# Kernel tuning notes

Measured on AMD Instinct MI355X. Metric: run time of the kernel, lower is better.

The kernel has to match this reference:

```python
import jax, jax.numpy as jnp
import numpy as np

BETA = 0.5

def setup_inputs() -> dict:
    key = jax.random.key(0)
    ks = jax.random.split(key, 10)
    B, H = 4096, 200
    ITEM, REGION = 100000, 1000
    D, HID = 128, 64  # embed_size, hidden_size
    half = D // 2
    history = jax.random.randint(ks[0], (B, H), 0, ITEM)
    target = jax.random.randint(ks[1], (B,), 0, ITEM)
    history_region = jax.random.randint(ks[2], (B, H), 0, REGION)
    target_region = jax.random.randint(ks[3], (B,), 0, REGION)
    W_hist = jax.random.normal(ks[4], (ITEM, half), jnp.float32) * 0.01
    W_tgt = jax.random.normal(ks[5], (ITEM, half), jnp.float32) * 0.01
    W_reg = jax.random.normal(ks[6], (REGION, half), jnp.float32) * 0.01
    W1 = jax.random.normal(ks[7], (D, HID), jnp.float32) * (1.0 / np.sqrt(D))
    b1 = jnp.zeros((HID,), jnp.float32)
    W2 = jax.random.normal(ks[8], (HID,), jnp.float32) * (1.0 / np.sqrt(HID))
    return {"history": history, "target": target,
            "history_region": history_region, "target_region": target_region,
            "W_hist": W_hist, "W_tgt": W_tgt, "W_reg": W_reg,
            "W1": W1, "b1": b1, "W2": W2}

def reference(history, target, history_region, target_region,
              W_hist, W_tgt, W_reg, W1, b1, W2):
    # gather + concat: [B,H,D] and [B,D]
    h = jnp.concatenate([W_hist[history], W_reg[history_region]], axis=-1)
    t = jnp.concatenate([W_tgt[target], W_reg[target_region]], axis=-1)
    inp = h * t[:, None, :]                      # [B,H,D]
    r1 = jax.nn.relu(inp @ W1 + b1)              # [B,H,HID] (dropout = identity at eval)
    logits = r1 @ W2                             # [B,H]
    mask = (history != target[:, None]).astype(logits.dtype)
    exp_A = jnp.exp(logits) * mask               # [B,H]
    exp_sum = jnp.sum(exp_A, axis=-1) ** BETA    # [B], beta-power normalization
    attn = exp_A / exp_sum[:, None]              # [B,H]
    pred = jnp.einsum('bhd,bd->b', h * attn[..., None], t)
    return jax.nn.sigmoid(pred)
```

## Files before the change

kernel.cpp:

```cpp
#include <hip/hip_runtime.h>
#include <math.h>

#define NB        4096
#define NH        200
#define HIST_ROWS 100000
#define REG_ROWS  1000
#define NTILES    13

typedef __attribute__((ext_vector_type(4))) int   int4i;

#define SA 2048.0f
#define SB 16384.0f
#define ST 2048.0f
#define INV_LOGIT (1.0f / (SA * SB))
#define INV_S     (1.0f / (SA * ST))

__device__ __forceinline__ int q8(float x, float s) {
    return __float2int_rn(fminf(fmaxf(x * s, -127.f), 127.f));
}
__device__ __forceinline__ int pack4(float a, float b, float c, float d, float s) {
    const int x0 = q8(a, s), x1 = q8(b, s), x2 = q8(c, s), x3 = q8(d, s);
    return (x0 & 255) | ((x1 & 255) << 8) | ((x2 & 255) << 16) | (x3 << 24);
}

__global__ __launch_bounds__(256) void prep_i8(
    const float* __restrict__ Wh, const float* __restrict__ Wr,
    const float* __restrict__ W1,
    unsigned char* __restrict__ tab, float* __restrict__ W1F2)
{
    for (int i = blockIdx.x * blockDim.x + threadIdx.x; i < 10240;
         i += gridDim.x * blockDim.x) {
        const int chunk = i >> 4, j = i & 15;
        const int frag = chunk >> 6, nt = frag >> 1, ks = frag & 1;
        const int c = chunk & 63, q = c >> 4, l = c & 15;
        W1F2[i] = (nt < 4) ? W1[(ks * 64 + q * 16 + j) * 64 + nt * 16 + l] : 0.f;
    }
    const int total = (HIST_ROWS + REG_ROWS) * 16;
    const int HE    = HIST_ROWS * 16;
    unsigned* dst = (unsigned*)tab;
    for (int i = blockIdx.x * blockDim.x + threadIdx.x; i < total;
         i += gridDim.x * blockDim.x) {
        const float4 v = (i < HE) ? ((const float4*)Wh)[i]
                                  : ((const float4*)Wr)[i - HE];
        dst[i] = (unsigned)pack4(v.x, v.y, v.z, v.w, SA);
    }
}

__global__ __launch_bounds__(256, 3) void nais_wl(
    const int*   __restrict__ history,
    const int*   __restrict__ target,
    const int*   __restrict__ history_region,
    const int*   __restrict__ target_region,
    const float* __restrict__ W_tgt,
    const float* __restrict__ W_reg,
    const float* __restrict__ b1,
    const float* __restrict__ W2,
    const unsigned char* __restrict__ tab,
    const float* __restrict__ W1F2,
    float*       __restrict__ out)
{
    __shared__ __align__(16) int Bw[4 * 640 * 4];

    const int tid  = threadIdx.x;
    const int lane = tid & 63, wv = tid >> 6;
    const int b    = blockIdx.x * 4 + wv;
    const int l15  = lane & 15, quad = lane >> 4;
    const int r_sel = l15 & 3;
    const int bNH  = b * NH;
    const int q16  = quad * 16;

    const int tgt  = target[b];
    const int treg = target_region[b];
    const float* tW = W_tgt + (size_t)tgt * 64;
    const float* rW = W_reg + (size_t)treg * 64;

    int4i*       Bst = (int4i*)Bw + wv * 640;
    const int4i* Bp  = (const int4i*)Bw + wv * 640;

    int4i sAh0, sAr0, sAh1, sAr1, sAh2, sAr2;
    int   mIh0, mIr0, mIh1, mIr1, mIh2, mIr2;

#define LOADIDX(S, T) do {                                                    \
        int j_ = (T) * 16 + l15;                                              \
        if (j_ >= NH) j_ = NH - 1;             \
        mIh##S = history[bNH + j_];                                           \
        mIr##S = history_region[bNH + j_];                                    \
    } while (0)

#define GATH(S) do {                                                          \
        sAh##S = *(const int4i*)(tab + (size_t)mIh##S * 64 + q16);            \
        sAr##S = *(const int4i*)(tab + (size_t)(HIST_ROWS + mIr##S) * 64 + q16); \
    } while (0)

    LOADIDX(0, 0); GATH(0);
    LOADIDX(1, 1); GATH(1);
    LOADIDX(2, 2); GATH(2);

    #pragma unroll
    for (int v = 0; v < 10; ++v) {
        const int ks = v & 1;
        const float4* tp = (const float4*)((ks ? rW : tW) + q16);
        const float4 t0 = tp[0], t1 = tp[1], t2 = tp[2], t3 = tp[3];
        int4i ob;
        if (v < 8) {
            const float4* wp = (const float4*)(W1F2 + (v * 64 + lane) * 16);
            const float4 w0 = wp[0], w1 = wp[1], w2 = wp[2], w3 = wp[3];
            ob.x = pack4(w0.x * t0.x, w0.y * t0.y, w0.z * t0.z, w0.w * t0.w, SB);
            ob.y = pack4(w1.x * t1.x, w1.y * t1.y, w1.z * t1.z, w1.w * t1.w, SB);
            ob.z = pack4(w2.x * t2.x, w2.y * t2.y, w2.z * t2.z, w2.w * t2.w, SB);
            ob.w = pack4(w3.x * t3.x, w3.y * t3.y, w3.z * t3.z, w3.w * t3.w, SB);
        } else {
            if (l15 == 0) {
                ob.x = pack4(t0.x, t0.y, t0.z, t0.w, ST);
                ob.y = pack4(t1.x, t1.y, t1.z, t1.w, ST);
                ob.z = pack4(t2.x, t2.y, t2.z, t2.w, ST);
                ob.w = pack4(t3.x, t3.y, t3.z, t3.w, ST);
            } else {
                ob = (int4i){0, 0, 0, 0};
            }
        }
        Bst[v * 64 + lane] = ob;
    }
    __syncthreads();

    const float w2_0 = W2[l15],      w2_1 = W2[16 + l15];
    const float w2_2 = W2[32 + l15], w2_3 = W2[48 + l15];
    const float b1_0 = b1[l15],      b1_1 = b1[16 + l15];
    const float b1_2 = b1[32 + l15], b1_3 = b1[48 + l15];

    float e_acc = 0.f, p_acc = 0.f;

#define EPINT(NT) do {                                                        \
        p0_ += fmaxf((float)acc##NT[0] * INV_LOGIT + b1_##NT, 0.f) * w2_##NT; \
        p1_ += fmaxf((float)acc##NT[1] * INV_LOGIT + b1_##NT, 0.f) * w2_##NT; \
        p2_ += fmaxf((float)acc##NT[2] * INV_LOGIT + b1_##NT, 0.f) * w2_##NT; \
        p3_ += fmaxf((float)acc##NT[3] * INV_LOGIT + b1_##NT, 0.f) * w2_##NT; \
    } while (0)
#define XR(P) do {                                                            \
        P += __shfl_xor(P, 1); P += __shfl_xor(P, 2);                         \
        P += __shfl_xor(P, 4); P += __shfl_xor(P, 8);                         \
    } while (0)

#define BODY(S, T) do {                                                       \
        asm volatile("" ::: "memory");                                        \
        const int4i bq0 = Bp[0 * 64 + lane], bq1 = Bp[1 * 64 + lane];         \
        const int4i bq2 = Bp[2 * 64 + lane], bq3 = Bp[3 * 64 + lane];         \
        const int4i bq4 = Bp[4 * 64 + lane], bq5 = Bp[5 * 64 + lane];         \
        const int4i bq6 = Bp[6 * 64 + lane], bq7 = Bp[7 * 64 + lane];         \
        const int4i bq8 = Bp[8 * 64 + lane], bq9 = Bp[9 * 64 + lane];         \
        int4i acc0 = {0,0,0,0}, acc1 = {0,0,0,0}, acc2 = {0,0,0,0};           \
        int4i acc3 = {0,0,0,0}, acc4 = {0,0,0,0};                             \
        acc0 = __builtin_amdgcn_mfma_i32_16x16x64_i8(sAh##S, bq0, acc0, 0, 0, 0); \
        acc1 = __builtin_amdgcn_mfma_i32_16x16x64_i8(sAh##S, bq2, acc1, 0, 0, 0); \
        acc2 = __builtin_amdgcn_mfma_i32_16x16x64_i8(sAh##S, bq4, acc2, 0, 0, 0); \
        acc3 = __builtin_amdgcn_mfma_i32_16x16x64_i8(sAh##S, bq6, acc3, 0, 0, 0); \
        acc4 = __builtin_amdgcn_mfma_i32_16x16x64_i8(sAh##S, bq8, acc4, 0, 0, 0); \
        acc0 = __builtin_amdgcn_mfma_i32_16x16x64_i8(sAr##S, bq1, acc0, 0, 0, 0); \
        acc1 = __builtin_amdgcn_mfma_i32_16x16x64_i8(sAr##S, bq3, acc1, 0, 0, 0); \
        acc2 = __builtin_amdgcn_mfma_i32_16x16x64_i8(sAr##S, bq5, acc2, 0, 0, 0); \
        acc3 = __builtin_amdgcn_mfma_i32_16x16x64_i8(sAr##S, bq7, acc3, 0, 0, 0); \
        acc4 = __builtin_amdgcn_mfma_i32_16x16x64_i8(sAr##S, bq9, acc4, 0, 0, 0); \
        float p0_ = 0.f, p1_ = 0.f, p2_ = 0.f, p3_ = 0.f;                     \
        EPINT(0); EPINT(1); EPINT(2); EPINT(3);                               \
        XR(p0_); XR(p1_); XR(p2_); XR(p3_);                                   \
        const float lgA_ = (r_sel & 1) ? p1_ : p0_;                           \
        const float lgB_ = (r_sel & 1) ? p3_ : p2_;                           \
        const float lg_  = (r_sel & 2) ? lgB_ : lgA_;                         \
        const float sv0_ = (float)__shfl(acc4[0], lane & 48);                 \
        const float sv1_ = (float)__shfl(acc4[1], lane & 48);                 \
        const float sv2_ = (float)__shfl(acc4[2], lane & 48);                 \
        const float sv3_ = (float)__shfl(acc4[3], lane & 48);                 \
        const float svA_ = (r_sel & 1) ? sv1_ : sv0_;                         \
        const float svB_ = (r_sel & 1) ? sv3_ : sv2_;                         \
        const float s_own_ = ((r_sel & 2) ? svB_ : svA_) * INV_S;             \
        const int  ihj_  = __shfl(mIh##S, quad * 4 + r_sel);                  \
        const int  jrow_ = (T) * 16 + quad * 4 + r_sel;                       \
        const bool valid_ = (l15 < 4) && (jrow_ < NH) && (ihj_ != tgt);       \
        const float ex_ = valid_ ? expf(lg_) : 0.f;                          \
        e_acc += ex_;                                                         \
        p_acc += ex_ * s_own_;                                                \
    } while (0)

    BODY(0, 0);   LOADIDX(0, 3);  GATH(0);
    BODY(1, 1);   LOADIDX(1, 4);  GATH(1);
    BODY(2, 2);   LOADIDX(2, 5);  GATH(2);
    BODY(0, 3);   LOADIDX(0, 6);  GATH(0);
    BODY(1, 4);   LOADIDX(1, 7);  GATH(1);
    BODY(2, 5);   LOADIDX(2, 8);  GATH(2);
    BODY(0, 6);   LOADIDX(0, 9);  GATH(0);
    BODY(1, 7);   LOADIDX(1, 10); GATH(1);
    BODY(2, 8);   LOADIDX(2, 11); GATH(2);
    BODY(0, 9);   LOADIDX(0, 12); GATH(0);
    BODY(1, 10);
    BODY(2, 11);
    BODY(0, 12);
#undef BODY
#undef EPINT
#undef XR
#undef GATH
#undef LOADIDX

    #pragma unroll
    for (int off = 1; off < 64; off <<= 1) {
        e_acc += __shfl_xor(e_acc, off);
        p_acc += __shfl_xor(p_acc, off);
    }
    if (lane == 0) {
        const float pred = p_acc / sqrtf(e_acc);
        out[b] = 1.f / (1.f + expf(-pred));
    }
}

__device__ __forceinline__ void epi_store_i8(
    const int4i* accT, const float* w2v, const float* b1v,
    int tl, int quad, int l15, float* logit_lds, float* s_lds)
{
    float part[4] = {0.f, 0.f, 0.f, 0.f};
    #pragma unroll
    for (int nt = 0; nt < 4; ++nt)
        #pragma unroll
        for (int r = 0; r < 4; ++r)
            part[r] += fmaxf((float)accT[nt][r] * INV_LOGIT + b1v[nt], 0.f) * w2v[nt];
    #pragma unroll
    for (int r = 0; r < 4; ++r) {
        part[r] += __shfl_xor(part[r], 1);
        part[r] += __shfl_xor(part[r], 2);
        part[r] += __shfl_xor(part[r], 4);
        part[r] += __shfl_xor(part[r], 8);
    }
    if (l15 == 0) {
        const int jg = tl * 16 + quad * 4;
        #pragma unroll
        for (int r = 0; r < 4; ++r) {
            logit_lds[jg + r] = part[r];
            s_lds[jg + r]     = (float)accT[4][r] * INV_S;
        }
    }
}

__device__ __forceinline__ int4i quant_row_fp32(const float* row, int quad) {
    const float4* p = (const float4*)(row + quad * 16);
    const float4 v0 = p[0], v1 = p[1], v2 = p[2], v3 = p[3];
    int4i o;
    o.x = pack4(v0.x, v0.y, v0.z, v0.w, SA);
    o.y = pack4(v1.x, v1.y, v1.z, v1.w, SA);
    o.z = pack4(v2.x, v2.y, v2.z, v2.w, SA);
    o.w = pack4(v3.x, v3.y, v3.z, v3.w, SA);
    return o;
}

__global__ __launch_bounds__(256, 3) void nais_fb(
    const int*   __restrict__ history,
    const int*   __restrict__ target,
    const int*   __restrict__ history_region,
    const int*   __restrict__ target_region,
    const float* __restrict__ W_hist,
    const float* __restrict__ W_tgt,
    const float* __restrict__ W_reg,
    const float* __restrict__ W1,
    const float* __restrict__ b1,
    const float* __restrict__ W2,
    float*       __restrict__ out)
{
    __shared__ int hist_lds[224];
    __shared__ int hreg_lds[224];
    __shared__ __align__(16) float t_lds[128];
    __shared__ __align__(16) int Bf4[640 * 4];
    __shared__ float logit_lds[208];
    __shared__ float s_lds[208];
    __shared__ float red_e[4], red_p[4];

    const int b   = blockIdx.x;
    const int tid = threadIdx.x;
    const int tgt = target[b];

    if (tid < 224) {
        const int jj = tid < NH ? tid : NH - 1;
        hist_lds[tid] = history[b * NH + jj];
        hreg_lds[tid] = history_region[b * NH + jj];
    }
    if (tid < 64) {
        t_lds[tid] = W_tgt[(size_t)tgt * 64 + tid];
    } else if (tid < 128) {
        t_lds[tid] = W_reg[(size_t)target_region[b] * 64 + (tid - 64)];
    }
    __syncthreads();

    const int lane = tid & 63, wv = tid >> 6;
    const int l15  = lane & 15, quad = lane >> 4;
    const int  tls[4] = {wv, wv + 4, wv + 8, wv + 12};
    const bool has3   = (tls[3] < NTILES);

    #pragma unroll
    for (int v = 0; v < 3; ++v) {
        const int i = tid + v * 256;
        if (i < 640) {
            const int frag = i >> 6, nt = frag >> 1, ks = frag & 1;
            const int c = i & 63, q = c >> 4, l = c & 15;
            const int k0 = ks * 64 + q * 16;
            const float4 t0 = *(const float4*)(t_lds + k0);
            const float4 t1 = *(const float4*)(t_lds + k0 + 4);
            const float4 t2 = *(const float4*)(t_lds + k0 + 8);
            const float4 t3 = *(const float4*)(t_lds + k0 + 12);
            int4i ob;
            if (nt < 4) {
                const int n = nt * 16 + l;
                float tmp[16];
                #pragma unroll
                for (int j = 0; j < 16; ++j) tmp[j] = W1[(k0 + j) * 64 + n];
                ob.x = pack4(tmp[0] * t0.x, tmp[1] * t0.y, tmp[2] * t0.z, tmp[3] * t0.w, SB);
                ob.y = pack4(tmp[4] * t1.x, tmp[5] * t1.y, tmp[6] * t1.z, tmp[7] * t1.w, SB);
                ob.z = pack4(tmp[8] * t2.x, tmp[9] * t2.y, tmp[10] * t2.z, tmp[11] * t2.w, SB);
                ob.w = pack4(tmp[12] * t3.x, tmp[13] * t3.y, tmp[14] * t3.z, tmp[15] * t3.w, SB);
            } else {
                if (l == 0) {
                    ob.x = pack4(t0.x, t0.y, t0.z, t0.w, ST);
                    ob.y = pack4(t1.x, t1.y, t1.z, t1.w, ST);
                    ob.z = pack4(t2.x, t2.y, t2.z, t2.w, ST);
                    ob.w = pack4(t3.x, t3.y, t3.z, t3.w, ST);
                } else {
                    ob = (int4i){0, 0, 0, 0};
                }
            }
            *reinterpret_cast<int4i*>(&Bf4[i * 4]) = ob;
        }
    }
    __syncthreads();

    float w2v[4], b1v[4];
    #pragma unroll
    for (int nt = 0; nt < 4; ++nt) {
        w2v[nt] = W2[nt * 16 + l15];
        b1v[nt] = b1[nt * 16 + l15];
    }

    int4i A[4][2];
    #pragma unroll
    for (int pp = 0; pp < 2; ++pp) {
        const int t0i = pp * 2, t1i = pp * 2 + 1;
        const bool hb = (t1i < 3) || has3;

        #pragma unroll
        for (int tt = 0; tt < 2; ++tt) {
            const int ti = t0i + tt;
            const int j  = ((ti == 3 && !has3) ? tls[2] : tls[ti]) * 16 + l15;
            A[ti][0] = quant_row_fp32(W_hist + (size_t)hist_lds[j] * 64, quad);
            A[ti][1] = quant_row_fp32(W_reg  + (size_t)hreg_lds[j] * 64, quad);
        }

        int4i acc[2][5];
        #pragma unroll
        for (int tt = 0; tt < 2; ++tt)
            #pragma unroll
            for (int nt = 0; nt < 5; ++nt) acc[tt][nt] = (int4i){0, 0, 0, 0};

        #pragma unroll
        for (int ks = 0; ks < 2; ++ks) {
            int4i bfr[5];
            #pragma unroll
            for (int nt = 0; nt < 5; ++nt)
                bfr[nt] = *reinterpret_cast<const int4i*>(&Bf4[((nt * 2 + ks) * 64 + lane) * 4]);
            #pragma unroll
            for (int nt = 0; nt < 5; ++nt)
                acc[0][nt] = __builtin_amdgcn_mfma_i32_16x16x64_i8(A[t0i][ks], bfr[nt], acc[0][nt], 0, 0, 0);
            if (hb) {
                #pragma unroll
                for (int nt = 0; nt < 5; ++nt)
                    acc[1][nt] = __builtin_amdgcn_mfma_i32_16x16x64_i8(A[t1i][ks], bfr[nt], acc[1][nt], 0, 0, 0);
            }
        }

        epi_store_i8(acc[0], w2v, b1v, tls[t0i], quad, l15, logit_lds, s_lds);
        if (hb) epi_store_i8(acc[1], w2v, b1v, tls[t1i], quad, l15, logit_lds, s_lds);
    }
    __syncthreads();

    float e = 0.f, p = 0.f;
    if (tid < NH) {
        const float ex = (hist_lds[tid] != tgt) ? expf(logit_lds[tid]) : 0.f;
        e = ex;
        p = ex * s_lds[tid];
    }
    #pragma unroll
    for (int off = 32; off > 0; off >>= 1) {
        e += __shfl_down(e, off);
        p += __shfl_down(p, off);
    }
    if (lane == 0) { red_e[wv] = e; red_p[wv] = p; }
    __syncthreads();
    if (tid == 0) {
        const float E = red_e[0] + red_e[1] + red_e[2] + red_e[3];
        const float P = red_p[0] + red_p[1] + red_p[2] + red_p[3];
        const float pred = P / sqrtf(E);
        out[b] = 1.f / (1.f + expf(-pred));
    }
}

extern "C" void kernel_launch(void* const* d_in, const int* in_sizes, int n_in,
                              void* d_out, int out_size, void* d_ws, size_t ws_size,
                              hipStream_t stream) {
    const int*   history        = (const int*)  d_in[0];
    const int*   target         = (const int*)  d_in[1];
    const int*   history_region = (const int*)  d_in[2];
    const int*   target_region  = (const int*)  d_in[3];
    const float* W_hist         = (const float*)d_in[4];
    const float* W_tgt          = (const float*)d_in[5];
    const float* W_reg          = (const float*)d_in[6];
    const float* W1             = (const float*)d_in[7];
    const float* b1             = (const float*)d_in[8];
    const float* W2             = (const float*)d_in[9];
    float* out = (float*)d_out;

    const size_t tab_bytes = (size_t)(HIST_ROWS + REG_ROWS) * 64;
    const size_t need = tab_bytes + 10240 * 4;
    if (ws_size >= need) {
        unsigned char* tab = (unsigned char*)d_ws;
        float* W1F2 = (float*)((char*)d_ws + tab_bytes);
        prep_i8<<<2048, 256, 0, stream>>>(W_hist, W_reg, W1, tab, W1F2);
        nais_wl<<<NB / 4, 256, 0, stream>>>(history, target, history_region, target_region,
                                            W_tgt, W_reg, b1, W2, tab, W1F2, out);
    } else {
        nais_fb<<<NB, 256, 0, stream>>>(history, target, history_region, target_region,
                                        W_hist, W_tgt, W_reg, W1, b1, W2, out);
    }
}
```

Baseline: 142.4 us.

## Split each batch row across two waves with shared B tile and LDS reduction

```diff
diff --git a/kernel.cpp b/kernel.cpp
--- a/kernel.cpp
+++ b/kernel.cpp
@@ -46,7 +46,7 @@
     }
 }
 
-__global__ __launch_bounds__(256, 3) void nais_wl(
+__global__ __launch_bounds__(256, 8) void nais_w2(
     const int*   __restrict__ history,
     const int*   __restrict__ target,
     const int*   __restrict__ history_region,
@@ -59,11 +59,12 @@
     const float* __restrict__ W1F2,
     float*       __restrict__ out)
 {
-    __shared__ __align__(16) int Bw[4 * 640 * 4];
+    __shared__ __align__(16) int Bw[2 * 640 * 4];
 
     const int tid  = threadIdx.x;
     const int lane = tid & 63, wv = tid >> 6;
-    const int b    = blockIdx.x * 4 + wv;
+    const int bh   = wv >> 1, par = wv & 1;
+    const int b    = blockIdx.x * 2 + bh;
     const int l15  = lane & 15, quad = lane >> 4;
     const int r_sel = l15 & 3;
     const int bNH  = b * NH;
@@ -74,11 +75,11 @@
     const float* tW = W_tgt + (size_t)tgt * 64;
     const float* rW = W_reg + (size_t)treg * 64;
 
-    int4i*       Bst = (int4i*)Bw + wv * 640;
-    const int4i* Bp  = (const int4i*)Bw + wv * 640;
-
-    int4i sAh0, sAr0, sAh1, sAr1, sAh2, sAr2;
-    int   mIh0, mIr0, mIh1, mIr1, mIh2, mIr2;
+    int4i*       Bst = (int4i*)Bw + bh * 640;
+    const int4i* Bp  = (const int4i*)Bw + bh * 640;
+
+    int4i sAh0, sAr0, sAh1, sAr1;
+    int   mIh0, mIr0, mIh1, mIr1;
 
 #define LOADIDX(S, T) do {                                                    \
         int j_ = (T) * 16 + l15;                                              \
@@ -92,18 +93,18 @@
         sAr##S = *(const int4i*)(tab + (size_t)(HIST_ROWS + mIr##S) * 64 + q16); \
     } while (0)
 
-    LOADIDX(0, 0); GATH(0);
-    LOADIDX(1, 1); GATH(1);
-    LOADIDX(2, 2); GATH(2);
-
-    #pragma unroll
-    for (int v = 0; v < 10; ++v) {
-        const int ks = v & 1;
+    LOADIDX(0, par);     GATH(0);
+    LOADIDX(1, par + 2); GATH(1);
+
+    #pragma unroll
+    for (int v = 0; v < 5; ++v) {
+        const int V  = par * 5 + v;
+        const int ks = V & 1;
         const float4* tp = (const float4*)((ks ? rW : tW) + q16);
         const float4 t0 = tp[0], t1 = tp[1], t2 = tp[2], t3 = tp[3];
         int4i ob;
-        if (v < 8) {
-            const float4* wp = (const float4*)(W1F2 + (v * 64 + lane) * 16);
+        if (V < 8) {
+            const float4* wp = (const float4*)(W1F2 + (V * 64 + lane) * 16);
             const float4 w0 = wp[0], w1 = wp[1], w2 = wp[2], w3 = wp[3];
             ob.x = pack4(w0.x * t0.x, w0.y * t0.y, w0.z * t0.z, w0.w * t0.w, SB);
             ob.y = pack4(w1.x * t1.x, w1.y * t1.y, w1.z * t1.z, w1.w * t1.w, SB);
@@ -119,7 +120,7 @@
                 ob = (int4i){0, 0, 0, 0};
             }
         }
-        Bst[v * 64 + lane] = ob;
+        Bst[V * 64 + lane] = ob;
     }
     __syncthreads();
 
@@ -141,8 +142,9 @@
         P += __shfl_xor(P, 4); P += __shfl_xor(P, 8);                         \
     } while (0)
 
-#define BODY(S, T) do {                                                       \
+#define BODY(S, K) do {                                                       \
         asm volatile("" ::: "memory");                                        \
+        const int T_ = 2 * (K) + par;                                         \
         const int4i bq0 = Bp[0 * 64 + lane], bq1 = Bp[1 * 64 + lane];         \
         const int4i bq2 = Bp[2 * 64 + lane], bq3 = Bp[3 * 64 + lane];         \
         const int4i bq4 = Bp[4 * 64 + lane], bq5 = Bp[5 * 64 + lane];         \
@@ -174,26 +176,20 @@
         const float svB_ = (r_sel & 1) ? sv3_ : sv2_;                         \
         const float s_own_ = ((r_sel & 2) ? svB_ : svA_) * INV_S;             \
         const int  ihj_  = __shfl(mIh##S, quad * 4 + r_sel);                  \
-        const int  jrow_ = (T) * 16 + quad * 4 + r_sel;                       \
+        const int  jrow_ = T_ * 16 + quad * 4 + r_sel;                        \
         const bool valid_ = (l15 < 4) && (jrow_ < NH) && (ihj_ != tgt);       \
         const float ex_ = valid_ ? expf(lg_) : 0.f;                          \
         e_acc += ex_;                                                         \
         p_acc += ex_ * s_own_;                                                \
     } while (0)
 
-    BODY(0, 0);   LOADIDX(0, 3);  GATH(0);
-    BODY(1, 1);   LOADIDX(1, 4);  GATH(1);
-    BODY(2, 2);   LOADIDX(2, 5);  GATH(2);
-    BODY(0, 3);   LOADIDX(0, 6);  GATH(0);
-    BODY(1, 4);   LOADIDX(1, 7);  GATH(1);
-    BODY(2, 5);   LOADIDX(2, 8);  GATH(2);
-    BODY(0, 6);   LOADIDX(0, 9);  GATH(0);
-    BODY(1, 7);   LOADIDX(1, 10); GATH(1);
-    BODY(2, 8);   LOADIDX(2, 11); GATH(2);
-    BODY(0, 9);   LOADIDX(0, 12); GATH(0);
-    BODY(1, 10);
-    BODY(2, 11);
-    BODY(0, 12);
+    BODY(0, 0);  LOADIDX(0, par + 4);  GATH(0);
+    BODY(1, 1);  LOADIDX(1, par + 6);  GATH(1);
+    BODY(0, 2);  LOADIDX(0, par + 8);  GATH(0);
+    BODY(1, 3);  LOADIDX(1, par + 10); GATH(1);
+    BODY(0, 4);  if (par == 0) { LOADIDX(0, 12); GATH(0); }
+    BODY(1, 5);
+    if (par == 0) { BODY(0, 6); }
 #undef BODY
 #undef EPINT
 #undef XR
@@ -205,8 +201,18 @@
         e_acc += __shfl_xor(e_acc, off);
         p_acc += __shfl_xor(p_acc, off);
     }
+
+    __syncthreads();
+    float* redm = (float*)Bw;
     if (lane == 0) {
-        const float pred = p_acc / sqrtf(e_acc);
+        redm[bh * 2 + par]     = e_acc;
+        redm[4 + bh * 2 + par] = p_acc;
+    }
+    __syncthreads();
+    if (par == 0 && lane == 0) {
+        const float E = redm[bh * 2]     + redm[bh * 2 + 1];
+        const float P = redm[4 + bh * 2] + redm[4 + bh * 2 + 1];
+        const float pred = P / sqrtf(E);
         out[b] = 1.f / (1.f + expf(-pred));
     }
 }
@@ -417,7 +423,7 @@
         unsigned char* tab = (unsigned char*)d_ws;
         float* W1F2 = (float*)((char*)d_ws + tab_bytes);
         prep_i8<<<2048, 256, 0, stream>>>(W_hist, W_reg, W1, tab, W1F2);
-        nais_wl<<<NB / 4, 256, 0, stream>>>(history, target, history_region, target_region,
+        nais_w2<<<NB / 2, 256, 0, stream>>>(history, target, history_region, target_region,
                                             W_tgt, W_reg, b1, W2, tab, W1F2, out);
     } else {
         nais_fb<<<NB, 256, 0, stream>>>(history, target, history_region, target_region,
```

Measured after the change: 234.2 us. +64.5%, slower.
